# Kernel tuning notes

Hardware: AMD Instinct MI355X
Metric: run time of the kernel (lower is better)

The kernel has to match this reference:

```python
import jax, jax.numpy as jnp
import numpy as np
from jax import lax

B, T, E, H, V = 1024, 128, 300, 100, 50000
K = 4  # topk in catch()
NEG_INF = -1e30


def setup_inputs() -> dict:
    key = jax.random.key(0)
    ks = jax.random.split(key, 12)
    word_id = jax.random.randint(ks[0], (B, T), 0, V, dtype=jnp.int32)
    sen_len = jax.random.randint(ks[1], (B,), K, T + 1, dtype=jnp.int32)  # >= K for topk
    label_word_id = jax.random.randint(ks[2], (B, 1), 0, V, dtype=jnp.int32)
    emb = jax.random.normal(ks[3], (V, E), jnp.float32) * 0.1
    W_ih = jax.random.normal(ks[4], (4 * H, E), jnp.float32) * 0.05
    W_hh = jax.random.normal(ks[5], (4 * H, H), jnp.float32) * 0.05
    b_ih = jax.random.normal(ks[6], (4 * H,), jnp.float32) * 0.05
    b_hh = jax.random.normal(ks[7], (4 * H,), jnp.float32) * 0.05
    lin_W = jax.random.normal(ks[8], (6, H), jnp.float32) * 0.1
    lin_b = jax.random.normal(ks[9], (6,), jnp.float32) * 0.1
    ll_W = jax.random.normal(ks[10], (H, E), jnp.float32) * 0.05
    ll_b = jax.random.normal(ks[11], (H,), jnp.float32) * 0.05
    return dict(word_id=word_id, sen_len=sen_len, label_word_id=label_word_id,
                emb=emb, W_ih=W_ih, W_hh=W_hh, b_ih=b_ih, b_hh=b_hh,
                lin_W=lin_W, lin_b=lin_b, ll_W=ll_W, ll_b=ll_b)


def _lstm(x, W_ih, W_hh, b_ih, b_hh):
    # x: (B, T, E) -> out: (B, T, H). Single layer, pytorch gate order i,f,g,o.
    b = b_ih + b_hh
    def step(carry, x_t):
        h, c = carry
        gates = x_t @ W_ih.T + h @ W_hh.T + b  # (B, 4H)
        i, f, g, o = jnp.split(gates, 4, axis=-1)
        c = jax.nn.sigmoid(f) * c + jax.nn.sigmoid(i) * jnp.tanh(g)
        h = jax.nn.sigmoid(o) * jnp.tanh(c)
        return (h, c), h
    h0 = jnp.zeros((x.shape[0], W_hh.shape[1]), x.dtype)
    (_, _), hs = lax.scan(step, (h0, h0), x.transpose(1, 0, 2))
    return hs.transpose(1, 0, 2)


def reference(word_id, sen_len, label_word_id, emb, W_ih, W_hh, b_ih, b_hh,
              lin_W, lin_b, ll_W, ll_b):
    word_vec = emb[word_id]                      # (B, T, E)
    out = _lstm(word_vec, W_ih, W_hh, b_ih, b_hh)  # (B, T, H)

    # last valid hidden state -> linear
    last = out[jnp.arange(out.shape[0]), sen_len - 1]  # (B, H)
    out_f = last @ lin_W.T + lin_b               # (B, 6)

    # label vector through llinear
    label_vec = emb[label_word_id[:, 0]] @ ll_W.T + ll_b  # (B, H)

    # --- catch(), vectorized ---
    scores = jnp.einsum('bth,bh->bt', out, label_vec)     # (B, T)
    valid = jnp.arange(out.shape[1])[None, :] < sen_len[:, None]  # (B, T)
    vals, idx = lax.top_k(jnp.where(valid, scores, NEG_INF), K)   # (B, K)
    s_value = jnp.take_along_axis(out, idx[:, :, None], axis=1)   # (B, K, H)
    pos = jnp.sum(s_value * vals[:, :, None], axis=1)             # (B, H)

    # neg: valid positions excluding topk; original bug: vector_list accumulates
    # across the batch loop -> cumulative sum over batch dimension.
    top_mask = jnp.zeros(valid.shape, bool).at[
        jnp.arange(valid.shape[0])[:, None], idx].set(True)
    neg_mask = valid & ~top_mask                                   # (B, T)
    per_neg = jnp.einsum('bth,bt->bh', out, neg_mask.astype(out.dtype))
    neg = jnp.cumsum(per_neg, axis=0)                              # (B, H)

    l_rep = pos @ lin_W.T + lin_b
    r_rep = neg @ lin_W.T + lin_b
    return (out_f, l_rep, r_rep)
```

## Files before the change

kernel.cpp:

```cpp
#include <hip/hip_runtime.h>
#include <hip/hip_bf16.h>
#include <cstdint>

#define Bn   1024
#define Tn   128
#define En   300
#define Hn   100
#define Vn   50000
#define G4n  400
#define MPn  50048
#define NPn  448

typedef __bf16 bf16x8 __attribute__((ext_vector_type(8)));
typedef _Float16 half8 __attribute__((ext_vector_type(8)));
typedef _Float16 half2v __attribute__((ext_vector_type(2)));
typedef float  f32x4  __attribute__((ext_vector_type(4)));

#define OFF_TABLE  0ull
#define OFF_WFRAG  44800000ull
#define OFF_WFRAGB 44914688ull
#define OFF_LLWT   45201408ull
#define OFF_LV     45321408ull
#define OFF_PN6    45731008ull

__device__ __forceinline__ float sigf(float x) {
    return __builtin_amdgcn_rcpf(1.0f + __expf(-x));
}
__device__ __forceinline__ float tanhfast(float x) {
    return 1.0f - 2.0f * __builtin_amdgcn_rcpf(__expf(2.0f * x) + 1.0f);
}

#define BAR_LDS() do {                                         \
    asm volatile("s_waitcnt lgkmcnt(0)" ::: "memory");          \
    __builtin_amdgcn_s_barrier();                               \
    asm volatile("" ::: "memory");                              \
} while (0)

#define DPP_ADD_SHL(v, N) do {                                                     \
    int _s = __builtin_amdgcn_update_dpp(0, __builtin_bit_cast(int, (v)),          \
                                         0x100 | (N), 0xF, 0xF, true);             \
    (v) += __builtin_bit_cast(float, _s);                                          \
} while (0)

__global__ void k_prep(const float* __restrict__ W_ih, const float* __restrict__ W_hh,
                       const float* __restrict__ llW,
                       uint4* __restrict__ wfrag, uint4* __restrict__ wfragB,
                       float* __restrict__ llwt) {
    int idx = blockIdx.x * 256 + threadIdx.x;
    if (idx < 28 * 4 * 64) {
        int lane = idx & 63, tk = idx >> 6;
        int nt = tk >> 2, kc = tk & 3;
        int n = nt * 16 + (lane & 15);
        int k0 = kc * 32 + (lane >> 4) * 8;
        int q = n & 3, u = n >> 2;
        union { _Float16 h[8]; uint4 v; } pk;
#pragma unroll
        for (int j = 0; j < 8; j++) {
            int k = k0 + j;
            pk.h[j] = (_Float16)((u < Hn && k < Hn) ? W_hh[(size_t)(q * Hn + u) * Hn + k] : 0.0f);
        }
        wfrag[idx] = pk.v;
    }
    if (idx < 10 * 28 * 64) {
        int lane = idx & 63, tk = idx >> 6;
        int kc = tk / 28, nsg = tk - kc * 28;
        int n = nsg * 16 + (lane & 15);
        int k0 = kc * 32 + (lane >> 4) * 8;
        int q = n & 3, u = n >> 2;
        union { __bf16 h[8]; uint4 v; } pk;
#pragma unroll
        for (int j = 0; j < 8; j++) {
            int k = k0 + j;
            pk.h[j] = (__bf16)((u < Hn && k < En) ? W_ih[(size_t)(q * Hn + u) * En + k] : 0.0f);
        }
        wfragB[idx] = pk.v;
    }
    if (idx < En * Hn) {
        int k = idx / Hn, h = idx - k * Hn;
        llwt[idx] = llW[(size_t)h * En + k];
    }
}

__global__ __launch_bounds__(256, 2) void k_table(
    const float* __restrict__ emb, const uint4* __restrict__ wfragB,
    const float* __restrict__ b_ih, const float* __restrict__ b_hh,
    _Float16* __restrict__ table) {
    __shared__ __bf16 a_sh[64][328];
    const int tid = threadIdx.x;
    const int mt = blockIdx.x >> 1, nh = blockIdx.x & 1;

#pragma unroll
    for (int it = 0; it < 5; it++) {
        int x = it * 256 + tid;
        int row = x / 20, seg = x - row * 20;
        int gr = mt * 64 + row;
        const float* ar = emb + (size_t)(gr < Vn ? gr : Vn - 1) * En;
        int c0 = seg * 16;
        union { __bf16 h[16]; bf16x8 v[2]; } pk;
#pragma unroll
        for (int g = 0; g < 4; g++) {
            int c = c0 + g * 4;
            if (c + 4 <= En) {
                float4 f = *(const float4*)(ar + c);
                pk.h[g * 4 + 0] = (__bf16)f.x; pk.h[g * 4 + 1] = (__bf16)f.y;
                pk.h[g * 4 + 2] = (__bf16)f.z; pk.h[g * 4 + 3] = (__bf16)f.w;
            } else {
                pk.h[g * 4 + 0] = (__bf16)0.f; pk.h[g * 4 + 1] = (__bf16)0.f;
                pk.h[g * 4 + 2] = (__bf16)0.f; pk.h[g * 4 + 3] = (__bf16)0.f;
            }
        }
        *(bf16x8*)&a_sh[row][c0] = pk.v[0];
        *(bf16x8*)&a_sh[row][c0 + 8] = pk.v[1];
    }
    __syncthreads();

    const int wv = tid >> 6, l = tid & 63;
    const int c16 = l & 15, quad = l >> 4;
    f32x4 acc[14];
#pragma unroll
    for (int i = 0; i < 14; i++) acc[i] = (f32x4){0.f, 0.f, 0.f, 0.f};

    uint4 bcur[14];
#pragma unroll
    for (int ns = 0; ns < 14; ns++) bcur[ns] = wfragB[((0 * 28 + nh * 14 + ns) << 6) + l];

    for (int kc = 0; kc < 10; kc++) {
        uint4 bnxt[14];
        if (kc < 9) {
#pragma unroll
            for (int ns = 0; ns < 14; ns++) bnxt[ns] = wfragB[(((kc + 1) * 28 + nh * 14 + ns) << 6) + l];
        }
        bf16x8 af = *(const bf16x8*)&a_sh[wv * 16 + c16][kc * 32 + quad * 8];
#pragma unroll
        for (int ns = 0; ns < 14; ns++)
            acc[ns] = __builtin_amdgcn_mfma_f32_16x16x32_bf16(af, __builtin_bit_cast(bf16x8, bcur[ns]), acc[ns], 0, 0, 0);
        if (kc < 9) {
#pragma unroll
            for (int ns = 0; ns < 14; ns++) bcur[ns] = bnxt[ns];
        }
    }
#pragma unroll
    for (int ns = 0; ns < 14; ns++) {
        int n = (nh * 14 + ns) * 16 + c16;
        int q = n & 3, u = n >> 2;
        if (u < Hn) {
            int j = q * Hn + u;
            float bias = b_ih[j] + b_hh[j];
#pragma unroll
            for (int r = 0; r < 4; r++) {
                int m = mt * 64 + wv * 16 + quad * 4 + r;
                if (m < Vn) table[(size_t)m * NPn + n] = (_Float16)(acc[ns][r] + bias);
            }
        }
    }
}

__global__ void k_label(const int* __restrict__ lwid, const float* __restrict__ emb,
                        const float* __restrict__ llwt, const float* __restrict__ llb,
                        float* __restrict__ lv) {
    __shared__ float er[En];
    __shared__ float part[Hn];
    int b = blockIdx.x;
    int lid = lwid[b];
    for (int k = threadIdx.x; k < En; k += 256) er[k] = emb[(size_t)lid * En + k];
    __syncthreads();
    int h = threadIdx.x & 127, half = threadIdx.x >> 7;
    float acc = 0.f;
    if (h < Hn) {
        int k0 = half * 150, k1 = k0 + 150;
        for (int k = k0; k < k1; k++) acc += er[k] * llwt[k * Hn + h];
        if (half == 1) part[h] = acc;
    }
    __syncthreads();
    if (h < Hn && half == 0) lv[(size_t)b * Hn + h] = acc + part[h] + llb[h];
}

__global__ __launch_bounds__(256, 2) void k_lstm(
    const int* __restrict__ word_id, const int* __restrict__ sen_len,
    const _Float16* __restrict__ table, const uint4* __restrict__ wfrag,
    const float* __restrict__ lv, const float* __restrict__ linW,
    const float* __restrict__ linb, float* __restrict__ pn6,
    float* __restrict__ d_out) {
    __shared__ float    gbufs[4][280];
    __shared__ _Float16 h_cur[2][2][136];
    __shared__ _Float16 oh_lds[2][12832];
    __shared__ float    spw[2][Tn][16];
    __shared__ int      widc[2][Tn];
    __shared__ float    pos_sh[2][Hn];
    __shared__ float    lasth_sh[2][Hn];
    __shared__ float    neg_sh[2][Hn];
    __shared__ float    tk_val[2][4];
    __shared__ int      tk_idx[2][4];

    const int tid = threadIdx.x;
    const int w = tid >> 6, l = tid & 63;
    const int c16 = l & 15, quad = l >> 4;
    const int b0 = blockIdx.x * 2;

    for (int i = tid; i < 272; i += 256) ((uint32_t*)h_cur)[i] = 0u;
    { int imb = tid >> 7, it = tid & 127; widc[imb][it] = word_id[(b0 + imb) * Tn + it] * NPn; }

    half8 bfr[7][4];
#pragma unroll
    for (int n7 = 0; n7 < 7; n7++)
#pragma unroll
        for (int kc = 0; kc < 4; kc++)
            bfr[n7][kc] = __builtin_bit_cast(half8, wfrag[((w * 7 + n7) * 4 + kc) * 64 + l]);

    const int u_loc = l >> 1, mb = l & 1;
    const int u = w * 28 + u_loc;
    const bool act = (l < 56) && (u < Hn);
    const int myslen = act ? sen_len[b0 + mb] : 0;
    const float lt_reg = act ? lv[(size_t)(b0 + mb) * Hn + u] : 0.f;
    float* gb = &gbufs[w][0];
    const _Float16* tb_u = table + u * 4;

    __syncthreads();

    uint2 xq = {0, 0}, xq1 = {0, 0};
    if (act) {
        xq  = *(const uint2*)(tb_u + (size_t)widc[mb][0]);
        xq1 = *(const uint2*)(tb_u + (size_t)widc[mb][1]);
    }

    float c_reg = 0.f, sumh = 0.f, lasth = 0.f;
    float p_carry = 0.f;

    for (int t = 0; t < Tn; t++) {
        const _Float16* hp = &h_cur[t & 1][0][0];
        f32x4 acc[7];
        {
            half8 af0 = *(const half8*)(hp + (c16 & 1) * 136 + quad * 8);
#pragma unroll
            for (int n7 = 0; n7 < 7; n7++)
                acc[n7] = __builtin_amdgcn_mfma_f32_16x16x32_f16(
                    af0, bfr[n7][0], (f32x4){0.f, 0.f, 0.f, 0.f}, 0, 0, 0);
        }
#pragma unroll
        for (int kc = 1; kc < 4; kc++) {
            half8 af = *(const half8*)(hp + (c16 & 1) * 136 + kc * 32 + quad * 8);
#pragma unroll
            for (int n7 = 0; n7 < 7; n7++)
                acc[n7] = __builtin_amdgcn_mfma_f32_16x16x32_f16(af, bfr[n7][kc], acc[n7], 0, 0, 0);
        }
        if (l < 16) {
#pragma unroll
            for (int n7 = 0; n7 < 7; n7++) {
                int nl = n7 * 16 + l;
                int adr = (nl >> 2) * 5 + (nl & 3);
                gb[adr] = acc[n7][0];
                gb[140 + adr] = acc[n7][1];
            }
        }
        {
            float pr = p_carry;
            DPP_ADD_SHL(pr, 2);
            DPP_ADD_SHL(pr, 4);
            DPP_ADD_SHL(pr, 8);
            if ((l & 15) < 2 && t > 0) spw[l & 1][t - 1][w * 4 + quad] = pr;
        }
        float p = 0.f;
        if (act) {
            int base = mb * 140 + u_loc * 5;
            half2v x01 = __builtin_bit_cast(half2v, xq.x);
            half2v x23 = __builtin_bit_cast(half2v, xq.y);
            float gi = gb[base] + (float)x01.x;
            float gf = gb[base + 1] + (float)x01.y;
            float gg = gb[base + 2] + (float)x23.x;
            float go = gb[base + 3] + (float)x23.y;
            float c = sigf(gf) * c_reg + sigf(gi) * tanhfast(gg);
            c_reg = c;
            float hh = sigf(go) * tanhfast(c);
            _Float16 h16 = (_Float16)hh;
            h_cur[(t + 1) & 1][mb][u] = h16;
            oh_lds[mb][t * Hn + u] = h16;
            if (t < myslen) sumh += hh;
            if (t == myslen - 1) lasth = hh;
            p = hh * lt_reg;
            int tn2 = (t + 2 < Tn) ? t + 2 : Tn - 1;
            xq = xq1;
            xq1 = *(const uint2*)(tb_u + (size_t)widc[mb][tn2]);
        }
        p_carry = p;
        BAR_LDS();
    }
    {
        float pr = p_carry;
        DPP_ADD_SHL(pr, 2);
        DPP_ADD_SHL(pr, 4);
        DPP_ADD_SHL(pr, 8);
        if ((l & 15) < 2) spw[l & 1][Tn - 1][w * 4 + quad] = pr;
    }
    __syncthreads();
    if (w < 2) {
        int kmb = w, lane = l;
        int sl = sen_len[b0 + kmb];
        const float* s16a = &spw[kmb][lane][0];
        const float* s16b = &spw[kmb][lane + 64][0];
        float4 a0 = *(const float4*)(s16a + 0), a1 = *(const float4*)(s16a + 4);
        float4 a2 = *(const float4*)(s16a + 8), a3 = *(const float4*)(s16a + 12);
        float4 b0v = *(const float4*)(s16b + 0), b1v = *(const float4*)(s16b + 4);
        float4 b2v = *(const float4*)(s16b + 8), b3v = *(const float4*)(s16b + 12);
        float sa = (a0.x + a0.y + a0.z + a0.w) + (a1.x + a1.y + a1.z + a1.w)
                 + (a2.x + a2.y + a2.z + a2.w) + (a3.x + a3.y + a3.z + a3.w);
        float sb = (b0v.x + b0v.y + b0v.z + b0v.w) + (b1v.x + b1v.y + b1v.z + b1v.w)
                 + (b2v.x + b2v.y + b2v.z + b2v.w) + (b3v.x + b3v.y + b3v.z + b3v.w);
        float s0 = (lane < sl) ? sa : -1e30f;
        float s1 = (lane + 64 < sl) ? sb : -1e30f;
        bool tk0 = false, tk1 = false;
#pragma unroll
        for (int p4 = 0; p4 < 4; p4++) {
            float v = tk0 ? -1e30f : s0;
            int ix = lane;
            float v1 = tk1 ? -1e30f : s1;
            if (v1 > v) { v = v1; ix = lane + 64; }
            for (int off = 32; off; off >>= 1) {
                float ov = __shfl_down(v, off, 64);
                int oi = __shfl_down(ix, off, 64);
                if (ov > v || (ov == v && oi < ix)) { v = ov; ix = oi; }
            }
            v = __shfl(v, 0, 64);
            ix = __shfl(ix, 0, 64);
            if (lane == 0) { tk_val[kmb][p4] = v; tk_idx[kmb][p4] = ix; }
            if (ix == lane) tk0 = true;
            if (ix == lane + 64) tk1 = true;
        }
    }
    __syncthreads();
    if (act) {
        float pos = 0.f, nsum = sumh;
#pragma unroll
        for (int p4 = 0; p4 < 4; p4++) {
            int ix = tk_idx[mb][p4];
            float r = (float)oh_lds[mb][ix * Hn + u];
            pos += tk_val[mb][p4] * r;
            nsum -= r;
        }
        pos_sh[mb][u] = pos;
        lasth_sh[mb][u] = lasth;
        neg_sh[mb][u] = nsum;
    }
    __syncthreads();
    if (tid < 36) {
        int which = tid / 12, r = tid - which * 12;
        int pmb = r / 6, o = r - pmb * 6;
        const float* src = (which == 0) ? &lasth_sh[pmb][0]
                         : (which == 1) ? &pos_sh[pmb][0] : &neg_sh[pmb][0];
        float acc2 = (which == 2) ? 0.f : linb[o];
        for (int uu = 0; uu < Hn; uu++) acc2 += src[uu] * linW[o * Hn + uu];
        if (which == 0)      d_out[(b0 + pmb) * 6 + o] = acc2;
        else if (which == 1) d_out[Bn * 6 + (b0 + pmb) * 6 + o] = acc2;
        else                 pn6[(b0 + pmb) * 6 + o] = acc2;
    }
}

__global__ __launch_bounds__(1024) void k_scan6(const float* __restrict__ pn6,
                                                const float* __restrict__ linb,
                                                float* __restrict__ d_out) {
    __shared__ float wsum[16];
    __shared__ float wpre[16];
    int o = blockIdx.x, t = threadIdx.x;
    int lane = t & 63, wv = t >> 6;
    float v = pn6[t * 6 + o];
#pragma unroll
    for (int off = 1; off < 64; off <<= 1) {
        float x = __shfl_up(v, off, 64);
        if (lane >= off) v += x;
    }
    if (lane == 63) wsum[wv] = v;
    __syncthreads();
    if (t < 16) {
        float s = wsum[t];
#pragma unroll
        for (int off = 1; off < 16; off <<= 1) {
            float x = __shfl_up(s, off, 64);
            if (t >= off) s += x;
        }
        wpre[t] = s;
    }
    __syncthreads();
    float pre = wv ? wpre[wv - 1] : 0.f;
    d_out[2 * Bn * 6 + t * 6 + o] = v + pre + linb[o];
}

extern "C" void kernel_launch(void* const* d_in, const int* in_sizes, int n_in,
                              void* d_out, int out_size, void* d_ws, size_t ws_size,
                              hipStream_t stream) {
    const int*   word_id = (const int*)d_in[0];
    const int*   sen_len = (const int*)d_in[1];
    const int*   lwid    = (const int*)d_in[2];
    const float* emb     = (const float*)d_in[3];
    const float* W_ih    = (const float*)d_in[4];
    const float* W_hh    = (const float*)d_in[5];
    const float* b_ih    = (const float*)d_in[6];
    const float* b_hh    = (const float*)d_in[7];
    const float* linW    = (const float*)d_in[8];
    const float* linb    = (const float*)d_in[9];
    const float* llW     = (const float*)d_in[10];
    const float* llb     = (const float*)d_in[11];

    char* ws = (char*)d_ws;
    _Float16* table  = (_Float16*)(ws + OFF_TABLE);
    uint4*    wfrag  = (uint4*)(ws + OFF_WFRAG);
    uint4*    wfragB = (uint4*)(ws + OFF_WFRAGB);
    float*    llwt   = (float*)(ws + OFF_LLWT);
    float*    lvp    = (float*)(ws + OFF_LV);
    float*    pn6    = (float*)(ws + OFF_PN6);
    float*    outp   = (float*)d_out;

    k_prep<<<118, 256, 0, stream>>>(W_ih, W_hh, llW, wfrag, wfragB, llwt);
    k_table<<<(MPn / 64) * 2, 256, 0, stream>>>(emb, wfragB, b_ih, b_hh, table);
    k_label<<<Bn, 256, 0, stream>>>(lwid, emb, llwt, llb, lvp);
    k_lstm<<<Bn / 2, 256, 0, stream>>>(word_id, sen_len, table, wfrag, lvp, linW, linb, pn6, outp);
    k_scan6<<<6, 1024, 0, stream>>>(pn6, linb, outp);
}
```

Baseline: 278.8 us.

## Process four sequences per LSTM block with eight waves splitting gate tiles

The LSTM kernel moves from 2 sequences and 4 waves per block to 4 sequences and 8 waves per block, launching half as many blocks. Each wave now owns 3 or 4 MFMA gate tiles instead of 7, which shortens the per-timestep serial MFMA chain on the recurrent critical path. The gate buffer layout, score reduction (DPP plus shuffles) and top-k stage are reworked for 4 batch rows per block. The cost is more waves per step barrier and higher LDS use per block (oh_lds doubles), which may reduce the number of blocks resident per CU.

```diff
diff --git a/kernel.cpp b/kernel.cpp
--- a/kernel.cpp
+++ b/kernel.cpp
@@ -175,42 +175,49 @@
     if (h < Hn && half == 0) lv[(size_t)b * Hn + h] = acc + part[h] + llb[h];
 }
 
-__global__ __launch_bounds__(256, 2) void k_lstm(
+__global__ __launch_bounds__(512, 2) void k_lstm(
     const int* __restrict__ word_id, const int* __restrict__ sen_len,
     const _Float16* __restrict__ table, const uint4* __restrict__ wfrag,
     const float* __restrict__ lv, const float* __restrict__ linW,
     const float* __restrict__ linb, float* __restrict__ pn6,
     float* __restrict__ d_out) {
-    __shared__ float    gbufs[4][280];
-    __shared__ _Float16 h_cur[2][2][136];
-    __shared__ _Float16 oh_lds[2][12832];
-    __shared__ float    spw[2][Tn][16];
-    __shared__ int      widc[2][Tn];
-    __shared__ float    pos_sh[2][Hn];
-    __shared__ float    lasth_sh[2][Hn];
-    __shared__ float    neg_sh[2][Hn];
-    __shared__ float    tk_val[2][4];
-    __shared__ int      tk_idx[2][4];
+    __shared__ __align__(16) float    gbufs[8][320];
+    __shared__ __align__(16) _Float16 h_cur[2][4][144];
+    __shared__ __align__(16) _Float16 oh_lds[4][12832];
+    __shared__ __align__(16) float    spw[4][Tn][8];
+    __shared__ int      widc[4][Tn];
+    __shared__ float    pos_sh[4][Hn];
+    __shared__ float    lasth_sh[4][Hn];
+    __shared__ float    neg_sh[4][Hn];
+    __shared__ float    tk_val[4][4];
+    __shared__ int      tk_idx[4][4];
 
     const int tid = threadIdx.x;
     const int w = tid >> 6, l = tid & 63;
     const int c16 = l & 15, quad = l >> 4;
-    const int b0 = blockIdx.x * 2;
-
-    for (int i = tid; i < 272; i += 256) ((uint32_t*)h_cur)[i] = 0u;
+    const int b0 = blockIdx.x * 4;
+
+    for (int i = tid; i < 576; i += 512) ((uint32_t*)h_cur)[i] = 0u;
     { int imb = tid >> 7, it = tid & 127; widc[imb][it] = word_id[(b0 + imb) * Tn + it] * NPn; }
 
-    half8 bfr[7][4];
-#pragma unroll
-    for (int n7 = 0; n7 < 7; n7++)
-#pragma unroll
-        for (int kc = 0; kc < 4; kc++)
-            bfr[n7][kc] = __builtin_bit_cast(half8, wfrag[((w * 7 + n7) * 4 + kc) * 64 + l]);
-
-    const int u_loc = l >> 1, mb = l & 1;
-    const int u = w * 28 + u_loc;
-    const bool act = (l < 56) && (u < Hn);
-    const int myslen = act ? sen_len[b0 + mb] : 0;
+    const bool has4 = (w == 0);
+    const int TB = has4 ? 0 : 4 + 3 * (w - 1);
+    const int UB = TB * 4;
+    const int ITEMS = has4 ? 16 : 12;
+
+    half8 bfr[4][4];
+#pragma unroll
+    for (int kc = 0; kc < 4; kc++) {
+        bfr[0][kc] = __builtin_bit_cast(half8, wfrag[((TB + 0) * 4 + kc) * 64 + l]);
+        bfr[1][kc] = __builtin_bit_cast(half8, wfrag[((TB + 1) * 4 + kc) * 64 + l]);
+        bfr[2][kc] = __builtin_bit_cast(half8, wfrag[((TB + 2) * 4 + kc) * 64 + l]);
+        if (has4) bfr[3][kc] = __builtin_bit_cast(half8, wfrag[((TB + 3) * 4 + kc) * 64 + l]);
+    }
+
+    const int iu = l >> 2, mb = l & 3;
+    const int u = UB + iu;
+    const bool act = (iu < ITEMS);
+    const int slen = act ? sen_len[b0 + mb] : 0;
     const float lt_reg = act ? lv[(size_t)(b0 + mb) * Hn + u] : 0.f;
     float* gb = &gbufs[w][0];
     const _Float16* tb_u = table + u * 4;
@@ -228,40 +235,46 @@
 
     for (int t = 0; t < Tn; t++) {
         const _Float16* hp = &h_cur[t & 1][0][0];
-        f32x4 acc[7];
+        f32x4 acc[4];
         {
-            half8 af0 = *(const half8*)(hp + (c16 & 1) * 136 + quad * 8);
-#pragma unroll
-            for (int n7 = 0; n7 < 7; n7++)
-                acc[n7] = __builtin_amdgcn_mfma_f32_16x16x32_f16(
-                    af0, bfr[n7][0], (f32x4){0.f, 0.f, 0.f, 0.f}, 0, 0, 0);
+            half8 af0 = *(const half8*)(hp + (c16 & 3) * 144 + quad * 8);
+            acc[0] = __builtin_amdgcn_mfma_f32_16x16x32_f16(af0, bfr[0][0], (f32x4){0.f, 0.f, 0.f, 0.f}, 0, 0, 0);
+            acc[1] = __builtin_amdgcn_mfma_f32_16x16x32_f16(af0, bfr[1][0], (f32x4){0.f, 0.f, 0.f, 0.f}, 0, 0, 0);
+            acc[2] = __builtin_amdgcn_mfma_f32_16x16x32_f16(af0, bfr[2][0], (f32x4){0.f, 0.f, 0.f, 0.f}, 0, 0, 0);
+            if (has4) acc[3] = __builtin_amdgcn_mfma_f32_16x16x32_f16(af0, bfr[3][0], (f32x4){0.f, 0.f, 0.f, 0.f}, 0, 0, 0);
         }
 #pragma unroll
         for (int kc = 1; kc < 4; kc++) {
-            half8 af = *(const half8*)(hp + (c16 & 1) * 136 + kc * 32 + quad * 8);
-#pragma unroll
-            for (int n7 = 0; n7 < 7; n7++)
-                acc[n7] = __builtin_amdgcn_mfma_f32_16x16x32_f16(af, bfr[n7][kc], acc[n7], 0, 0, 0);
+            half8 af = *(const half8*)(hp + (c16 & 3) * 144 + kc * 32 + quad * 8);
+            acc[0] = __builtin_amdgcn_mfma_f32_16x16x32_f16(af, bfr[0][kc], acc[0], 0, 0, 0);
+            acc[1] = __builtin_amdgcn_mfma_f32_16x16x32_f16(af, bfr[1][kc], acc[1], 0, 0, 0);
+            acc[2] = __builtin_amdgcn_mfma_f32_16x16x32_f16(af, bfr[2][kc], acc[2], 0, 0, 0);
+            if (has4) acc[3] = __builtin_amdgcn_mfma_f32_16x16x32_f16(af, bfr[3][kc], acc[3], 0, 0, 0);
         }
         if (l < 16) {
-#pragma unroll
-            for (int n7 = 0; n7 < 7; n7++) {
-                int nl = n7 * 16 + l;
-                int adr = (nl >> 2) * 5 + (nl & 3);
-                gb[adr] = acc[n7][0];
-                gb[140 + adr] = acc[n7][1];
+            int adr0 = (c16 >> 2) * 5 + (c16 & 3);
+#pragma unroll
+            for (int r = 0; r < 4; r++) gb[r * 80 + adr0] = acc[0][r];
+#pragma unroll
+            for (int r = 0; r < 4; r++) gb[r * 80 + adr0 + 20] = acc[1][r];
+#pragma unroll
+            for (int r = 0; r < 4; r++) gb[r * 80 + adr0 + 40] = acc[2][r];
+            if (has4) {
+#pragma unroll
+                for (int r = 0; r < 4; r++) gb[r * 80 + adr0 + 60] = acc[3][r];
             }
         }
         {
             float pr = p_carry;
-            DPP_ADD_SHL(pr, 2);
             DPP_ADD_SHL(pr, 4);
             DPP_ADD_SHL(pr, 8);
-            if ((l & 15) < 2 && t > 0) spw[l & 1][t - 1][w * 4 + quad] = pr;
+            pr += __shfl_down(pr, 32, 64);
+            pr += __shfl_down(pr, 16, 64);
+            if (l < 4 && t > 0) spw[l][t - 1][w] = pr;
         }
         float p = 0.f;
         if (act) {
-            int base = mb * 140 + u_loc * 5;
+            int base = mb * 80 + iu * 5;
             half2v x01 = __builtin_bit_cast(half2v, xq.x);
             half2v x23 = __builtin_bit_cast(half2v, xq.y);
             float gi = gb[base] + (float)x01.x;
@@ -274,8 +287,8 @@
             _Float16 h16 = (_Float16)hh;
             h_cur[(t + 1) & 1][mb][u] = h16;
             oh_lds[mb][t * Hn + u] = h16;
-            if (t < myslen) sumh += hh;
-            if (t == myslen - 1) lasth = hh;
+            if (t < slen) sumh += hh;
+            if (t == slen - 1) lasth = hh;
             p = hh * lt_reg;
             int tn2 = (t + 2 < Tn) ? t + 2 : Tn - 1;
             xq = xq1;
@@ -286,34 +299,30 @@
     }
     {
         float pr = p_carry;
-        DPP_ADD_SHL(pr, 2);
         DPP_ADD_SHL(pr, 4);
         DPP_ADD_SHL(pr, 8);
-        if ((l & 15) < 2) spw[l & 1][Tn - 1][w * 4 + quad] = pr;
-    }
-    __syncthreads();
-    if (w < 2) {
-        int kmb = w, lane = l;
-        int sl = sen_len[b0 + kmb];
-        const float* s16a = &spw[kmb][lane][0];
-        const float* s16b = &spw[kmb][lane + 64][0];
-        float4 a0 = *(const float4*)(s16a + 0), a1 = *(const float4*)(s16a + 4);
-        float4 a2 = *(const float4*)(s16a + 8), a3 = *(const float4*)(s16a + 12);
-        float4 b0v = *(const float4*)(s16b + 0), b1v = *(const float4*)(s16b + 4);
-        float4 b2v = *(const float4*)(s16b + 8), b3v = *(const float4*)(s16b + 12);
-        float sa = (a0.x + a0.y + a0.z + a0.w) + (a1.x + a1.y + a1.z + a1.w)
-                 + (a2.x + a2.y + a2.z + a2.w) + (a3.x + a3.y + a3.z + a3.w);
-        float sb = (b0v.x + b0v.y + b0v.z + b0v.w) + (b1v.x + b1v.y + b1v.z + b1v.w)
-                 + (b2v.x + b2v.y + b2v.z + b2v.w) + (b3v.x + b3v.y + b3v.z + b3v.w);
-        float s0 = (lane < sl) ? sa : -1e30f;
-        float s1 = (lane + 64 < sl) ? sb : -1e30f;
+        pr += __shfl_down(pr, 32, 64);
+        pr += __shfl_down(pr, 16, 64);
+        if (l < 4) spw[l][Tn - 1][w] = pr;
+    }
+    __syncthreads();
+    if (w < 4) {
+        int sl = sen_len[b0 + w];
+        float4 a0 = *(const float4*)&spw[w][l][0];
+        float4 a1 = *(const float4*)&spw[w][l][4];
+        float4 c0 = *(const float4*)&spw[w][l + 64][0];
+        float4 c1 = *(const float4*)&spw[w][l + 64][4];
+        float sa = (a0.x + a0.y + a0.z + a0.w) + (a1.x + a1.y + a1.z + a1.w);
+        float sb = (c0.x + c0.y + c0.z + c0.w) + (c1.x + c1.y + c1.z + c1.w);
+        float s0 = (l < sl) ? sa : -1e30f;
+        float s1 = (l + 64 < sl) ? sb : -1e30f;
         bool tk0 = false, tk1 = false;
 #pragma unroll
         for (int p4 = 0; p4 < 4; p4++) {
             float v = tk0 ? -1e30f : s0;
-            int ix = lane;
+            int ix = l;
             float v1 = tk1 ? -1e30f : s1;
-            if (v1 > v) { v = v1; ix = lane + 64; }
+            if (v1 > v) { v = v1; ix = l + 64; }
             for (int off = 32; off; off >>= 1) {
                 float ov = __shfl_down(v, off, 64);
                 int oi = __shfl_down(ix, off, 64);
@@ -321,9 +330,9 @@
             }
             v = __shfl(v, 0, 64);
             ix = __shfl(ix, 0, 64);
-            if (lane == 0) { tk_val[kmb][p4] = v; tk_idx[kmb][p4] = ix; }
-            if (ix == lane) tk0 = true;
-            if (ix == lane + 64) tk1 = true;
+            if (l == 0) { tk_val[w][p4] = v; tk_idx[w][p4] = ix; }
+            if (ix == l) tk0 = true;
+            if (ix == l + 64) tk1 = true;
         }
     }
     __syncthreads();
@@ -341,8 +350,8 @@
         neg_sh[mb][u] = nsum;
     }
     __syncthreads();
-    if (tid < 36) {
-        int which = tid / 12, r = tid - which * 12;
+    if (tid < 72) {
+        int which = tid / 24, r = tid - which * 24;
         int pmb = r / 6, o = r - pmb * 6;
         const float* src = (which == 0) ? &lasth_sh[pmb][0]
                          : (which == 1) ? &pos_sh[pmb][0] : &neg_sh[pmb][0];
@@ -411,6 +420,6 @@
     k_prep<<<118, 256, 0, stream>>>(W_ih, W_hh, llW, wfrag, wfragB, llwt);
     k_table<<<(MPn / 64) * 2, 256, 0, stream>>>(emb, wfragB, b_ih, b_hh, table);
     k_label<<<Bn, 256, 0, stream>>>(lwid, emb, llwt, llb, lvp);
-    k_lstm<<<Bn / 2, 256, 0, stream>>>(word_id, sen_len, table, wfrag, lvp, linW, linb, pn6, outp);
+    k_lstm<<<Bn / 4, 512, 0, stream>>>(word_id, sen_len, table, wfrag, lvp, linW, linb, pn6, outp);
     k_scan6<<<6, 1024, 0, stream>>>(pn6, linb, outp);
 }
```

Measured after the change: 294.0 us. 1.05x slower.
